# Optimization experiments

Measured on AMD Instinct MI355X. Metric: run time of the kernel, lower is better.

Reference implementation:

```python
import jax, jax.numpy as jnp
import numpy as np

HIDDEN = 768
FF = 3072
N_HEADS = 12
HEAD = HIDDEN // N_HEADS
WIDTH = 512  # attention window (number of attended keys, causal)
B, S = 2, 4096
EPS = 1e-6


def _rotary_sincos(seq_len, dim):
    # GPT-J style: freqs per pair, each value repeated twice (interleaved)
    inv_freq = 1.0 / (10000.0 ** (np.arange(0, dim, 2, dtype=np.float32) / dim))
    t = np.arange(seq_len, dtype=np.float32)
    ang = np.einsum('s,d->sd', t, inv_freq)              # [S, dim/2]
    ang = np.repeat(ang, 2, axis=-1)                     # [S, dim]
    return jnp.asarray(np.sin(ang))[:, None, :], jnp.asarray(np.cos(ang))[:, None, :]


def setup_inputs() -> dict:
    key = jax.random.key(0)
    ks = jax.random.split(key, 4)
    x = jax.random.normal(ks[0], (B, S, HIDDEN), dtype=jnp.float32)
    sin, cos = _rotary_sincos(S, HEAD)                   # [S,1,HEAD] each
    W_in = jax.random.normal(ks[1], (HIDDEN, 3 * HIDDEN + FF), dtype=jnp.float32) / np.sqrt(HIDDEN)
    b_in = jnp.zeros((3 * HIDDEN + FF,), dtype=jnp.float32)
    W_out = jax.random.normal(ks[2], (HIDDEN + FF, HIDDEN), dtype=jnp.float32) / np.sqrt(HIDDEN + FF)
    b_out = jnp.zeros((HIDDEN,), dtype=jnp.float32)
    w_norm = jnp.ones((HIDDEN,), dtype=jnp.float32)
    return {"x": x, "sin": sin, "cos": cos, "w_norm": w_norm,
            "W_in": W_in, "b_in": b_in, "W_out": W_out, "b_out": b_out}


def _rotate_every_two(x):
    x1 = x[..., ::2]
    x2 = x[..., 1::2]
    return jnp.stack((-x2, x1), axis=-1).reshape(x.shape)


def _apply_rope(x, sin, cos):
    # x: [B,S,H,hd]; sin/cos: [S,1,hd] -> broadcast as [1,S,1,hd]
    sin = sin[None]
    cos = cos[None]
    return x * cos + _rotate_every_two(x) * sin


def _windowed_attention(q, k, v, width):
    # q,k,v: [B,S,H,hd]; causal local attention: key j valid iff 0 <= i-j < width
    b, s, h, d = q.shape
    wb = width  # block size == window; each query block attends blocks (b-1, b)
    nb = s // wb
    scale = 1.0 / np.sqrt(d)
    qb = q.reshape(b, nb, wb, h, d)
    kp = jnp.pad(k, ((0, 0), (wb, 0), (0, 0), (0, 0))).reshape(b, nb + 1, wb, h, d)
    vp = jnp.pad(v, ((0, 0), (wb, 0), (0, 0), (0, 0))).reshape(b, nb + 1, wb, h, d)
    kb = jnp.concatenate([kp[:, :-1], kp[:, 1:]], axis=2)   # [B,nb,2wb,H,hd]
    vb = jnp.concatenate([vp[:, :-1], vp[:, 1:]], axis=2)
    scores = jnp.einsum('bnqhd,bnkhd->bnhqk', qb, kb) * scale
    qi = jnp.arange(wb)
    ki = jnp.arange(2 * wb)
    bi = jnp.arange(nb)
    diff = wb + qi[:, None] - ki[None, :]                    # i - j per block
    base = (diff >= 0) & (diff < width)                      # [wb, 2wb]
    valid_j = (bi[:, None, None] >= 1) | (ki[None, None, :] >= wb)  # j >= 0
    mask = base[None] & valid_j                              # [nb, wb, 2wb]
    neg = jnp.finfo(scores.dtype).min
    scores = jnp.where(mask[None, :, None], scores, neg)
    p = jax.nn.softmax(scores, axis=-1)
    out = jnp.einsum('bnhqk,bnkhd->bnqhd', p, vb)
    return out.reshape(b, s, h * d)


def reference(x, sin, cos, w_norm, W_in, b_in, W_out, b_out):
    # RMSNorm
    ms = jnp.mean(x * x, axis=-1, keepdims=True)
    xn = x * jax.lax.rsqrt(ms + EPS) * w_norm
    # fused QKV + FF projection
    t = xn @ W_in + b_in                                     # [B,S,3*HIDDEN+FF]
    ff = t[:, :, -FF:]
    qkv = t[:, :, :-FF].reshape(x.shape[0], x.shape[1], 3, N_HEADS, HEAD)
    q = _apply_rope(qkv[:, :, 0], sin, cos)
    k = _apply_rope(qkv[:, :, 1], sin, cos)
    v = qkv[:, :, 2]
    attn = _windowed_attention(q, k, v, WIDTH)               # [B,S,HIDDEN]
    ff = jax.nn.gelu(ff, approximate=False)
    combined = jnp.concatenate((attn, ff), axis=-1)          # [B,S,HIDDEN+FF]
    return combined @ W_out + b_out
```

## Files before the change

kernel.cpp:

```cpp
#include <hip/hip_runtime.h>
#include <hip/hip_bf16.h>

typedef short bf16x8 __attribute__((ext_vector_type(8)));
typedef float f32x4 __attribute__((ext_vector_type(4)));

#define LOG2E 1.4426950408889634f
#define QKV_E ((size_t)24*4096*64)

__device__ __forceinline__ float bfu2f(unsigned short u) {
  unsigned v = ((unsigned)u) << 16;
  return __builtin_bit_cast(float, v);
}
__device__ __forceinline__ unsigned short f2bfu(float f) {
  unsigned u = __builtin_bit_cast(unsigned, f);
  u += 0x7fffu + ((u >> 16) & 1u);
  return (unsigned short)(u >> 16);
}
__device__ __forceinline__ unsigned packbf2(float lo, float hi) {
  return (unsigned)f2bfu(lo) | ((unsigned)f2bfu(hi) << 16);
}
__device__ __forceinline__ float gelu_f(float v) {
  float a = fabsf(v) * 0.70710678118654752f;
  float t = 1.0f / (1.0f + 0.3275911f * a);
  float poly = ((((1.061405429f * t - 1.453152027f) * t + 1.421413741f) * t
                 - 0.284496736f) * t + 0.254829592f) * t;
  float erfa = 1.0f - poly * __expf(-a * a);
  float erfv = v >= 0.0f ? erfa : -erfa;
  return 0.5f * v * (1.0f + erfv);
}
__device__ __forceinline__ void gl_lds16(const ushort* g, ushort* l) {
  __builtin_amdgcn_global_load_lds(
      (const __attribute__((address_space(1))) unsigned int*)(const void*)g,
      (__attribute__((address_space(3))) unsigned int*)(void*)l, 16, 0, 0);
}

__global__ __launch_bounds__(256) void rmsnorm_k(const float* __restrict__ x,
    const float* __restrict__ w, ushort* __restrict__ xn) {
  int row = blockIdx.x, t = threadIdx.x;
  const float* xr = x + (size_t)row * 768;
  float v0 = xr[t], v1 = xr[t + 256], v2 = xr[t + 512];
  float ss = v0 * v0 + v1 * v1 + v2 * v2;
#pragma unroll
  for (int m = 32; m >= 1; m >>= 1) ss += __shfl_xor(ss, m, 64);
  __shared__ float part[4];
  if ((t & 63) == 0) part[t >> 6] = ss;
  __syncthreads();
  float tot = part[0] + part[1] + part[2] + part[3];
  float rr = rsqrtf(tot * (1.0f / 768.0f) + 1e-6f);
  ushort* xo = xn + (size_t)row * 768;
  xo[t]       = f2bfu(v0 * rr * w[t]);
  xo[t + 256] = f2bfu(v1 * rr * w[t + 256]);
  xo[t + 512] = f2bfu(v2 * rr * w[t + 512]);
}

__global__ __launch_bounds__(256) void tcvt_k(const float* __restrict__ in,
    ushort* __restrict__ out, int R, int C) {
  __shared__ float tile[32][33];
  int c0 = blockIdx.x * 32, r0 = blockIdx.y * 32;
  int t = threadIdx.x;
  int j = t & 31, i0 = t >> 5;
#pragma unroll
  for (int i = i0; i < 32; i += 8) tile[i][j] = in[(size_t)(r0 + i) * C + c0 + j];
  __syncthreads();
#pragma unroll
  for (int i = i0; i < 32; i += 8) out[(size_t)(c0 + i) * R + r0 + j] = f2bfu(tile[j][i]);
}

__global__ __launch_bounds__(256) void gemm1_k(const ushort* __restrict__ A,
    const ushort* __restrict__ Bt, const float* __restrict__ bias,
    const float* __restrict__ sn, const float* __restrict__ cs,
    ushort* __restrict__ qbuf, ushort* __restrict__ kbuf,
    ushort* __restrict__ vt, ushort* __restrict__ comb) {
  __shared__ __align__(16) ushort lds[2][2][128 * 64];
  const int t = threadIdx.x, lane = t & 63, w = t >> 6;
  const int wr = w >> 1, wc = w & 1;
  int bid = blockIdx.x;
  int n = (bid & 7) * 336 + (bid >> 3);
  int bx = n % 42, by = n / 42;
  const int mBase = by * 128, nBase = bx * 128;

  size_t gA[4], gB[4];
  int ldst[4];
#pragma unroll
  for (int j = 0; j < 4; ++j) {
    int row = w * 32 + j * 8 + (lane >> 3);
    int gc = ((lane & 7) ^ (lane >> 3)) * 8;
    gA[j] = (size_t)(mBase + row) * 768 + gc;
    gB[j] = (size_t)(nBase + row) * 768 + gc;
    ldst[j] = (w * 32 + j * 8) * 64;
  }

  f32x4 acc[4][4];
  f32x4 z = {0.f, 0.f, 0.f, 0.f};
#pragma unroll
  for (int m = 0; m < 4; ++m)
#pragma unroll
    for (int nn = 0; nn < 4; ++nn) acc[m][nn] = z;

#pragma unroll
  for (int j = 0; j < 4; ++j) {
    gl_lds16(A + gA[j], &lds[0][0][0] + ldst[j]);
    gl_lds16(Bt + gB[j], &lds[0][1][0] + ldst[j]);
  }
  __syncthreads();

#pragma unroll 1
  for (int kt = 0; kt < 12; ++kt) {
    const int cur = kt & 1;
    if (kt < 11) {
      int k0 = (kt + 1) * 64;
#pragma unroll
      for (int j = 0; j < 4; ++j) {
        gl_lds16(A + gA[j] + k0, &lds[1 - cur][0][0] + ldst[j]);
        gl_lds16(Bt + gB[j] + k0, &lds[1 - cur][1][0] + ldst[j]);
      }
    }
    const ushort* As = &lds[cur][0][0];
    const ushort* Bs = &lds[cur][1][0];
#pragma unroll
    for (int kk = 0; kk < 2; ++kk) {
      bf16x8 af[4], bff[4];
#pragma unroll
      for (int m = 0; m < 4; ++m) {
        int row = wr * 64 + m * 16 + (lane & 15);
        int slot = (kk * 4 + (lane >> 4)) ^ (lane & 7);
        af[m] = *(const bf16x8*)(As + row * 64 + slot * 8);
      }
#pragma unroll
      for (int nn = 0; nn < 4; ++nn) {
        int row = wc * 64 + nn * 16 + (lane & 15);
        int slot = (kk * 4 + (lane >> 4)) ^ (lane & 7);
        bff[nn] = *(const bf16x8*)(Bs + row * 64 + slot * 8);
      }
#pragma unroll
      for (int m = 0; m < 4; ++m)
#pragma unroll
        for (int nn = 0; nn < 4; ++nn)
          acc[m][nn] = __builtin_amdgcn_mfma_f32_16x16x32_bf16(bff[nn], af[m], acc[m][nn], 0, 0, 0);
    }
    __syncthreads();
  }

  const bool isff = (nBase >= 2304);
  const int region = nBase / 768;
#pragma unroll
  for (int m = 0; m < 4; ++m) {
    int row = mBase + wr * 64 + m * 16 + (lane & 15);
    int b = row >> 12, s = row & 4095;
#pragma unroll
    for (int nn = 0; nn < 4; ++nn) {
      int col = nBase + wc * 64 + nn * 16 + ((lane >> 4) << 2);
      f32x4 v = acc[m][nn] + *(const f32x4*)(bias + col);
      if (isff) {
        ushort4 o;
        o.x = f2bfu(gelu_f(v[0]));
        o.y = f2bfu(gelu_f(v[1]));
        o.z = f2bfu(gelu_f(v[2]));
        o.w = f2bfu(gelu_f(v[3]));
        *(ushort4*)(comb + (size_t)row * 3840 + (col - 1536)) = o;
      } else {
        int rem = col - region * 768;
        int h = rem >> 6, d0 = rem & 63;
        if (region == 2) {
          int l = s & 127;
          int pnn = l >> 4, pg = (l >> 2) & 3, pr = l & 3;
          int sp = (s & ~127) | (((pnn >> 1) * 4 + pg) * 8 + (pnn & 1) * 4 + pr);
          size_t vb = (size_t)((b * 12 + h) * 64 + d0) * 4096 + sp;
          vt[vb]          = f2bfu(v[0]);
          vt[vb + 4096]   = f2bfu(v[1]);
          vt[vb + 2*4096] = f2bfu(v[2]);
          vt[vb + 3*4096] = f2bfu(v[3]);
        } else {
          f32x4 sv = *(const f32x4*)(sn + (s << 6) + d0);
          f32x4 cv = *(const f32x4*)(cs + (s << 6) + d0);
          float o0 = v[0] * cv[0] - v[1] * sv[0];
          float o1 = v[1] * cv[0] + v[0] * sv[0];
          float o2 = v[2] * cv[2] - v[3] * sv[2];
          float o3 = v[3] * cv[2] + v[2] * sv[2];
          ushort4 o;
          if (region == 0) {
            o.x = f2bfu(o0 * 0.125f); o.y = f2bfu(o1 * 0.125f);
            o.z = f2bfu(o2 * 0.125f); o.w = f2bfu(o3 * 0.125f);
            *(ushort4*)(qbuf + ((size_t)((b * 12 + h) * 4096 + s)) * 64 + d0) = o;
          } else {
            o.x = f2bfu(o0); o.y = f2bfu(o1); o.z = f2bfu(o2); o.w = f2bfu(o3);
            *(ushort4*)(kbuf + ((size_t)((b * 12 + h) * 4096 + s)) * 64 + d0) = o;
          }
        }
      }
    }
  }
}

__global__ __launch_bounds__(512) void gemm2_k(const ushort* __restrict__ A,
    const ushort* __restrict__ Bt, const float* __restrict__ bias,
    float* __restrict__ out) {
  __shared__ __align__(16) ushort lds[2][2][2][128 * 64];
  const int t = threadIdx.x;
  const int grp = t >> 8, tl = t & 255;
  const int lane = tl & 63, w4 = tl >> 6;
  const int wr = w4 >> 1, wc = w4 & 1;
  int bid = blockIdx.x;
  int n = (bid & 7) * 48 + (bid >> 3);
  int bx = n % 6, by = n / 6;
  const int mBase = by * 128, nBase = bx * 128;
  const int kOff = grp * 1920;

  size_t gA[4], gB[4];
  int ldst[4];
#pragma unroll
  for (int j = 0; j < 4; ++j) {
    int row = w4 * 32 + j * 8 + (lane >> 3);
    int gc = ((lane & 7) ^ (lane >> 3)) * 8;
    gA[j] = (size_t)(mBase + row) * 3840 + kOff + gc;
    gB[j] = (size_t)(nBase + row) * 3840 + kOff + gc;
    ldst[j] = (w4 * 32 + j * 8) * 64;
  }

  f32x4 acc[4][4];
  f32x4 z = {0.f, 0.f, 0.f, 0.f};
#pragma unroll
  for (int m = 0; m < 4; ++m)
#pragma unroll
    for (int nn = 0; nn < 4; ++nn) acc[m][nn] = z;

#pragma unroll
  for (int j = 0; j < 4; ++j) {
    gl_lds16(A + gA[j], &lds[grp][0][0][0] + ldst[j]);
    gl_lds16(Bt + gB[j], &lds[grp][0][1][0] + ldst[j]);
  }
  __syncthreads();

#pragma unroll 1
  for (int kt = 0; kt < 30; ++kt) {
    const int cur = kt & 1;
    if (kt < 29) {
      int k0 = (kt + 1) * 64;
#pragma unroll
      for (int j = 0; j < 4; ++j) {
        gl_lds16(A + gA[j] + k0, &lds[grp][1 - cur][0][0] + ldst[j]);
        gl_lds16(Bt + gB[j] + k0, &lds[grp][1 - cur][1][0] + ldst[j]);
      }
    }
    const ushort* As = &lds[grp][cur][0][0];
    const ushort* Bs = &lds[grp][cur][1][0];
#pragma unroll
    for (int kk = 0; kk < 2; ++kk) {
      bf16x8 af[4], bff[4];
#pragma unroll
      for (int m = 0; m < 4; ++m) {
        int row = wr * 64 + m * 16 + (lane & 15);
        int slot = (kk * 4 + (lane >> 4)) ^ (lane & 7);
        af[m] = *(const bf16x8*)(As + row * 64 + slot * 8);
      }
#pragma unroll
      for (int nn = 0; nn < 4; ++nn) {
        int row = wc * 64 + nn * 16 + (lane & 15);
        int slot = (kk * 4 + (lane >> 4)) ^ (lane & 7);
        bff[nn] = *(const bf16x8*)(Bs + row * 64 + slot * 8);
      }
#pragma unroll
      for (int m = 0; m < 4; ++m)
#pragma unroll
        for (int nn = 0; nn < 4; ++nn)
          acc[m][nn] = __builtin_amdgcn_mfma_f32_16x16x32_bf16(bff[nn], af[m], acc[m][nn], 0, 0, 0);
    }
    __syncthreads();
  }

  f32x4* sc = (f32x4*)&lds[1][0][0][0];
  if (grp == 1) {
#pragma unroll
    for (int m = 0; m < 4; ++m)
#pragma unroll
      for (int nn = 0; nn < 4; ++nn) sc[tl * 16 + m * 4 + nn] = acc[m][nn];
  }
  __syncthreads();
  if (grp == 0) {
#pragma unroll
    for (int m = 0; m < 4; ++m) {
      int row = mBase + wr * 64 + m * 16 + (lane & 15);
#pragma unroll
      for (int nn = 0; nn < 4; ++nn) {
        int col = nBase + wc * 64 + nn * 16 + ((lane >> 4) << 2);
        f32x4 v = acc[m][nn] + sc[tl * 16 + m * 4 + nn] + *(const f32x4*)(bias + col);
        *(f32x4*)(out + (size_t)row * 768 + col) = v;
      }
    }
  }
}

__global__ __launch_bounds__(256, 2) void attn_k(const ushort* __restrict__ qb,
    const ushort* __restrict__ kb, const ushort* __restrict__ vt,
    ushort* __restrict__ comb) {
  __shared__ __align__(16) ushort KS[2][128 * 64];
  __shared__ __align__(16) ushort VS[2][64 * 128];
  int bid = blockIdx.x;
  int nb = (bid & 7) * 96 + (bid >> 3);
  int qt = nb & 31, bh = nb >> 5;
  const int t = threadIdx.x, lane = t & 63, w = t >> 6;
  const int g = lane >> 4, q15 = lane & 15;
  const int qlo = qt * 128;
  const size_t base = (size_t)bh * 4096 * 64;

  size_t kSrc[4], vSrc[4];
  int dstOff[4];
#pragma unroll
  for (int j = 0; j < 4; ++j) {
    int ck = (w * 4 + j) * 64 + lane;
    int key = ck >> 3, sl = ck & 7;
    kSrc[j] = (size_t)key * 64 + ((sl ^ (key & 7)) << 3);
    int dd = ck >> 4, s16 = ck & 15;
    vSrc[j] = (size_t)dd * 4096 + ((s16 ^ (dd & 15)) << 3);
    dstOff[j] = (w * 4 + j) * 512;
  }

  bf16x8 qa[2][2];
#pragma unroll
  for (int m = 0; m < 2; ++m)
#pragma unroll
    for (int kk = 0; kk < 2; ++kk) {
      int row = qlo + w * 32 + m * 16 + q15;
      qa[m][kk] = *(const bf16x8*)(qb + base + (size_t)row * 64 + kk * 32 + g * 8);
    }

  f32x4 z = {0.f, 0.f, 0.f, 0.f};
  f32x4 o[2][4];
#pragma unroll
  for (int m = 0; m < 2; ++m)
#pragma unroll
    for (int df = 0; df < 4; ++df) o[m][df] = z;
  float m_run[2] = {-1e30f, -1e30f}, l_run[2] = {0.f, 0.f};

  const int t0 = qt >= 4 ? qt - 4 : 0;
  const int nt = qt - t0 + 1;
  {
    int k0 = t0 * 128;
#pragma unroll
    for (int j = 0; j < 4; ++j) {
      gl_lds16(kb + base + (size_t)k0 * 64 + kSrc[j], &KS[0][0] + dstOff[j]);
      gl_lds16(vt + base + k0 + vSrc[j], &VS[0][0] + dstOff[j]);
    }
  }
  __syncthreads();

  const int qrow0 = qlo + w * 32 + q15;
#pragma unroll 1
  for (int it = 0; it < nt; ++it) {
    const int kt = t0 + it, k0 = kt * 128, cur = it & 1;
    if (it + 1 < nt) {
      int k1 = k0 + 128;
#pragma unroll
      for (int j = 0; j < 4; ++j) {
        gl_lds16(kb + base + (size_t)k1 * 64 + kSrc[j], &KS[1 - cur][0] + dstOff[j]);
        gl_lds16(vt + base + k1 + vSrc[j], &VS[1 - cur][0] + dstOff[j]);
      }
    }
    f32x4 s[2][8];
#pragma unroll
    for (int m = 0; m < 2; ++m)
#pragma unroll
      for (int nn = 0; nn < 8; ++nn) s[m][nn] = z;
#pragma unroll
    for (int kk = 0; kk < 2; ++kk) {
      bf16x8 kf[8];
#pragma unroll
      for (int nn = 0; nn < 8; ++nn) {
        int row = nn * 16 + q15;
        int slot = (kk * 4 + g) ^ (q15 & 7);
        kf[nn] = *(const bf16x8*)(&KS[cur][0] + row * 64 + slot * 8);
      }
#pragma unroll
      for (int m = 0; m < 2; ++m)
#pragma unroll
        for (int nn = 0; nn < 8; ++nn)
          s[m][nn] = __builtin_amdgcn_mfma_f32_16x16x32_bf16(kf[nn], qa[m][kk], s[m][nn], 0, 0, 0);
    }
    if (kt == qt) {
#pragma unroll
      for (int m = 0; m < 2; ++m) {
        int ql = qrow0 + m * 16 - k0;
#pragma unroll
        for (int nn = 0; nn < 8; ++nn)
#pragma unroll
          for (int r = 0; r < 4; ++r)
            if (nn * 16 + g * 4 + r > ql) s[m][nn][r] = -3e38f;
      }
    } else if (kt == qt - 4) {
#pragma unroll
      for (int m = 0; m < 2; ++m) {
        int ql = qrow0 + m * 16 - k0;
#pragma unroll
        for (int nn = 0; nn < 8; ++nn)
#pragma unroll
          for (int r = 0; r < 4; ++r)
            if (ql - (nn * 16 + g * 4 + r) >= 512) s[m][nn][r] = -3e38f;
      }
    }
    float mx[2];
    bool need = false;
#pragma unroll
    for (int m = 0; m < 2; ++m) {
      float v = s[m][0][0];
#pragma unroll
      for (int nn = 0; nn < 8; ++nn)
#pragma unroll
        for (int r = 0; r < 4; ++r) v = fmaxf(v, s[m][nn][r]);
      v = fmaxf(v, __shfl_xor(v, 16, 64));
      v = fmaxf(v, __shfl_xor(v, 32, 64));
      mx[m] = v;
      need |= (v > m_run[m] + 8.f);
    }
    if (__any(need)) {
#pragma unroll
      for (int m = 0; m < 2; ++m) {
        float mn = fmaxf(m_run[m], mx[m]);
        float sc = exp2f((m_run[m] - mn) * LOG2E);
        m_run[m] = mn;
        l_run[m] *= sc;
#pragma unroll
        for (int df = 0; df < 4; ++df) o[m][df] *= sc;
      }
    }
#pragma unroll
    for (int m = 0; m < 2; ++m) {
      float mr = m_run[m];
      float ls = 0.f;
#pragma unroll
      for (int nn = 0; nn < 8; ++nn)
#pragma unroll
        for (int r = 0; r < 4; ++r) {
          float p = exp2f((s[m][nn][r] - mr) * LOG2E);
          s[m][nn][r] = p;
          ls += p;
        }
      ls += __shfl_xor(ls, 16, 64);
      ls += __shfl_xor(ls, 32, 64);
      l_run[m] += ls;
    }
#pragma unroll
    for (int kk2 = 0; kk2 < 4; ++kk2) {
      bf16x8 pa[2];
#pragma unroll
      for (int m = 0; m < 2; ++m) {
        int4 pi4;
        pi4.x = (int)packbf2(s[m][2*kk2][0],   s[m][2*kk2][1]);
        pi4.y = (int)packbf2(s[m][2*kk2][2],   s[m][2*kk2][3]);
        pi4.z = (int)packbf2(s[m][2*kk2+1][0], s[m][2*kk2+1][1]);
        pi4.w = (int)packbf2(s[m][2*kk2+1][2], s[m][2*kk2+1][3]);
        pa[m] = __builtin_bit_cast(bf16x8, pi4);
      }
#pragma unroll
      for (int df = 0; df < 4; ++df) {
        int row = df * 16 + q15;
        int slot = (kk2 * 4 + g) ^ q15;
        bf16x8 vf = *(const bf16x8*)(&VS[cur][0] + row * 128 + slot * 8);
#pragma unroll
        for (int m = 0; m < 2; ++m)
          o[m][df] = __builtin_amdgcn_mfma_f32_16x16x32_bf16(vf, pa[m], o[m][df], 0, 0, 0);
      }
    }
    __syncthreads();
  }

  int b = bh / 12, h = bh % 12;
#pragma unroll
  for (int m = 0; m < 2; ++m) {
    float inv = 1.0f / l_run[m];
    int row = qrow0 + m * 16;
#pragma unroll
    for (int df = 0; df < 4; ++df) {
      ushort4 ov;
      ov.x = f2bfu(o[m][df][0] * inv);
      ov.y = f2bfu(o[m][df][1] * inv);
      ov.z = f2bfu(o[m][df][2] * inv);
      ov.w = f2bfu(o[m][df][3] * inv);
      *(ushort4*)(comb + (size_t)(b * 4096 + row) * 3840 + h * 64 + df * 16 + g * 4) = ov;
    }
  }
}

extern "C" void kernel_launch(void* const* d_in, const int* in_sizes, int n_in,
                              void* d_out, int out_size, void* d_ws, size_t ws_size,
                              hipStream_t stream) {
  (void)in_sizes; (void)n_in; (void)out_size; (void)ws_size;
  const float* x      = (const float*)d_in[0];
  const float* sin_t  = (const float*)d_in[1];
  const float* cos_t  = (const float*)d_in[2];
  const float* w_norm = (const float*)d_in[3];
  const float* W_in   = (const float*)d_in[4];
  const float* b_in   = (const float*)d_in[5];
  const float* W_out  = (const float*)d_in[6];
  const float* b_out  = (const float*)d_in[7];
  float* out = (float*)d_out;

  const size_t XN_E  = (size_t)8192 * 768;
  ushort* xn      = (ushort*)d_ws;
  ushort* qbuf    = xn + XN_E;
  ushort* kbuf    = qbuf + QKV_E;
  ushort* vt      = kbuf + QKV_E;
  ushort* w_in_t  = vt + QKV_E;
  ushort* w_out_t = w_in_t + (size_t)5376 * 768;
  ushort* comb    = w_out_t + (size_t)768 * 3840;

  rmsnorm_k<<<dim3(8192), dim3(256), 0, stream>>>(x, w_norm, xn);
  tcvt_k<<<dim3(5376 / 32, 768 / 32), dim3(256), 0, stream>>>(W_in, w_in_t, 768, 5376);
  tcvt_k<<<dim3(768 / 32, 3840 / 32), dim3(256), 0, stream>>>(W_out, w_out_t, 3840, 768);
  gemm1_k<<<dim3(2688), dim3(256), 0, stream>>>(xn, w_in_t, b_in, sin_t, cos_t,
                                                qbuf, kbuf, vt, comb);
  attn_k<<<dim3(768), dim3(256), 0, stream>>>(qbuf, kbuf, vt, comb);
  gemm2_k<<<dim3(384), dim3(512), 0, stream>>>(comb, w_out_t, b_out, out);
}
```

Baseline: 265.4 us.

## Overlap prefetch with compute via vmcnt waits, regroup tile mapping, drop gemm2 split-K

Replaces full __syncthreads in the double-buffered loops of gemm1, gemm2 and attention with explicit s_waitcnt vmcnt(8)/lgkmcnt(0) plus s_barrier. The async loads for the next tile can then stay in flight while the current tile is computed, instead of being drained at every barrier. Block-to-tile mapping for the GEMMs is changed to XCD-local groups for better L2 reuse, and gemm2 drops its intra-block split-K (512 threads, LDS reduction) for a 256-thread single-K kernel with occupancy hint 2. This trades parallelism per tile for lower LDS use and no reduction step, and it relies on the hand-counted vmcnt value being right.

```diff
diff --git a/kernel.cpp b/kernel.cpp
--- a/kernel.cpp
+++ b/kernel.cpp
@@ -33,6 +33,10 @@
       (const __attribute__((address_space(1))) unsigned int*)(const void*)g,
       (__attribute__((address_space(3))) unsigned int*)(void*)l, 16, 0, 0);
 }
+#define WAIT_VM8  asm volatile("s_waitcnt vmcnt(8)" ::: "memory")
+#define WAIT_VM0  asm volatile("s_waitcnt vmcnt(0)" ::: "memory")
+#define WAIT_LGKM asm volatile("s_waitcnt lgkmcnt(0)" ::: "memory")
+#define BAR       __builtin_amdgcn_s_barrier()
 
 __global__ __launch_bounds__(256) void rmsnorm_k(const float* __restrict__ x,
     const float* __restrict__ w, ushort* __restrict__ xn) {
@@ -66,7 +70,7 @@
   for (int i = i0; i < 32; i += 8) out[(size_t)(c0 + i) * R + r0 + j] = f2bfu(tile[j][i]);
 }
 
-__global__ __launch_bounds__(256) void gemm1_k(const ushort* __restrict__ A,
+__global__ __launch_bounds__(256, 2) void gemm1_k(const ushort* __restrict__ A,
     const ushort* __restrict__ Bt, const float* __restrict__ bias,
     const float* __restrict__ sn, const float* __restrict__ cs,
     ushort* __restrict__ qbuf, ushort* __restrict__ kbuf,
@@ -75,8 +79,10 @@
   const int t = threadIdx.x, lane = t & 63, w = t >> 6;
   const int wr = w >> 1, wc = w & 1;
   int bid = blockIdx.x;
-  int n = (bid & 7) * 336 + (bid >> 3);
-  int bx = n % 42, by = n / 42;
+  int xcd = bid & 7, local = bid >> 3;
+  int grp = local / 48, r6 = local % 48;
+  int bx = grp * 6 + r6 % 6;
+  int by = xcd * 8 + r6 / 6;
   const int mBase = by * 128, nBase = bx * 128;
 
   size_t gA[4], gB[4];
@@ -102,7 +108,6 @@
     gl_lds16(A + gA[j], &lds[0][0][0] + ldst[j]);
     gl_lds16(Bt + gB[j], &lds[0][1][0] + ldst[j]);
   }
-  __syncthreads();
 
 #pragma unroll 1
   for (int kt = 0; kt < 12; ++kt) {
@@ -114,7 +119,11 @@
         gl_lds16(A + gA[j] + k0, &lds[1 - cur][0][0] + ldst[j]);
         gl_lds16(Bt + gB[j] + k0, &lds[1 - cur][1][0] + ldst[j]);
       }
-    }
+      WAIT_VM8;
+    } else {
+      WAIT_VM0;
+    }
+    BAR;
     const ushort* As = &lds[cur][0][0];
     const ushort* Bs = &lds[cur][1][0];
 #pragma unroll
@@ -138,7 +147,8 @@
         for (int nn = 0; nn < 4; ++nn)
           acc[m][nn] = __builtin_amdgcn_mfma_f32_16x16x32_bf16(bff[nn], af[m], acc[m][nn], 0, 0, 0);
     }
-    __syncthreads();
+    WAIT_LGKM;
+    BAR;
   }
 
   const bool isff = (nBase >= 2304);
@@ -192,29 +202,28 @@
   }
 }
 
-__global__ __launch_bounds__(512) void gemm2_k(const ushort* __restrict__ A,
+__global__ __launch_bounds__(256, 2) void gemm2_k(const ushort* __restrict__ A,
     const ushort* __restrict__ Bt, const float* __restrict__ bias,
     float* __restrict__ out) {
-  __shared__ __align__(16) ushort lds[2][2][2][128 * 64];
-  const int t = threadIdx.x;
-  const int grp = t >> 8, tl = t & 255;
-  const int lane = tl & 63, w4 = tl >> 6;
-  const int wr = w4 >> 1, wc = w4 & 1;
+  __shared__ __align__(16) ushort lds[2][2][128 * 64];
+  const int t = threadIdx.x, lane = t & 63, w = t >> 6;
+  const int wr = w >> 1, wc = w & 1;
   int bid = blockIdx.x;
-  int n = (bid & 7) * 48 + (bid >> 3);
-  int bx = n % 6, by = n / 6;
+  int xcd = bid & 7, local = bid >> 3;
+  int g = local / 4, r4 = local % 4;
+  int bx = (g % 3) * 2 + (r4 & 1);
+  int by = xcd * 8 + (g / 3) * 2 + (r4 >> 1);
   const int mBase = by * 128, nBase = bx * 128;
-  const int kOff = grp * 1920;
 
   size_t gA[4], gB[4];
   int ldst[4];
 #pragma unroll
   for (int j = 0; j < 4; ++j) {
-    int row = w4 * 32 + j * 8 + (lane >> 3);
+    int row = w * 32 + j * 8 + (lane >> 3);
     int gc = ((lane & 7) ^ (lane >> 3)) * 8;
-    gA[j] = (size_t)(mBase + row) * 3840 + kOff + gc;
-    gB[j] = (size_t)(nBase + row) * 3840 + kOff + gc;
-    ldst[j] = (w4 * 32 + j * 8) * 64;
+    gA[j] = (size_t)(mBase + row) * 3840 + gc;
+    gB[j] = (size_t)(nBase + row) * 3840 + gc;
+    ldst[j] = (w * 32 + j * 8) * 64;
   }
 
   f32x4 acc[4][4];
@@ -226,24 +235,27 @@
 
 #pragma unroll
   for (int j = 0; j < 4; ++j) {
-    gl_lds16(A + gA[j], &lds[grp][0][0][0] + ldst[j]);
-    gl_lds16(Bt + gB[j], &lds[grp][0][1][0] + ldst[j]);
-  }
-  __syncthreads();
+    gl_lds16(A + gA[j], &lds[0][0][0] + ldst[j]);
+    gl_lds16(Bt + gB[j], &lds[0][1][0] + ldst[j]);
+  }
 
 #pragma unroll 1
-  for (int kt = 0; kt < 30; ++kt) {
+  for (int kt = 0; kt < 60; ++kt) {
     const int cur = kt & 1;
-    if (kt < 29) {
+    if (kt < 59) {
       int k0 = (kt + 1) * 64;
 #pragma unroll
       for (int j = 0; j < 4; ++j) {
-        gl_lds16(A + gA[j] + k0, &lds[grp][1 - cur][0][0] + ldst[j]);
-        gl_lds16(Bt + gB[j] + k0, &lds[grp][1 - cur][1][0] + ldst[j]);
-      }
-    }
-    const ushort* As = &lds[grp][cur][0][0];
-    const ushort* Bs = &lds[grp][cur][1][0];
+        gl_lds16(A + gA[j] + k0, &lds[1 - cur][0][0] + ldst[j]);
+        gl_lds16(Bt + gB[j] + k0, &lds[1 - cur][1][0] + ldst[j]);
+      }
+      WAIT_VM8;
+    } else {
+      WAIT_VM0;
+    }
+    BAR;
+    const ushort* As = &lds[cur][0][0];
+    const ushort* Bs = &lds[cur][1][0];
 #pragma unroll
     for (int kk = 0; kk < 2; ++kk) {
       bf16x8 af[4], bff[4];
@@ -265,27 +277,18 @@
         for (int nn = 0; nn < 4; ++nn)
           acc[m][nn] = __builtin_amdgcn_mfma_f32_16x16x32_bf16(bff[nn], af[m], acc[m][nn], 0, 0, 0);
     }
-    __syncthreads();
-  }
-
-  f32x4* sc = (f32x4*)&lds[1][0][0][0];
-  if (grp == 1) {
-#pragma unroll
-    for (int m = 0; m < 4; ++m)
-#pragma unroll
-      for (int nn = 0; nn < 4; ++nn) sc[tl * 16 + m * 4 + nn] = acc[m][nn];
-  }
-  __syncthreads();
-  if (grp == 0) {
-#pragma unroll
-    for (int m = 0; m < 4; ++m) {
-      int row = mBase + wr * 64 + m * 16 + (lane & 15);
-#pragma unroll
-      for (int nn = 0; nn < 4; ++nn) {
-        int col = nBase + wc * 64 + nn * 16 + ((lane >> 4) << 2);
-        f32x4 v = acc[m][nn] + sc[tl * 16 + m * 4 + nn] + *(const f32x4*)(bias + col);
-        *(f32x4*)(out + (size_t)row * 768 + col) = v;
-      }
+    WAIT_LGKM;
+    BAR;
+  }
+
+#pragma unroll
+  for (int m = 0; m < 4; ++m) {
+    int row = mBase + wr * 64 + m * 16 + (lane & 15);
+#pragma unroll
+    for (int nn = 0; nn < 4; ++nn) {
+      int col = nBase + wc * 64 + nn * 16 + ((lane >> 4) << 2);
+      f32x4 v = acc[m][nn] + *(const f32x4*)(bias + col);
+      *(f32x4*)(out + (size_t)row * 768 + col) = v;
     }
   }
 }
@@ -342,7 +345,6 @@
       gl_lds16(vt + base + k0 + vSrc[j], &VS[0][0] + dstOff[j]);
     }
   }
-  __syncthreads();
 
   const int qrow0 = qlo + w * 32 + q15;
 #pragma unroll 1
@@ -355,7 +357,11 @@
         gl_lds16(kb + base + (size_t)k1 * 64 + kSrc[j], &KS[1 - cur][0] + dstOff[j]);
         gl_lds16(vt + base + k1 + vSrc[j], &VS[1 - cur][0] + dstOff[j]);
       }
-    }
+      WAIT_VM8;
+    } else {
+      WAIT_VM0;
+    }
+    BAR;
     f32x4 s[2][8];
 #pragma unroll
     for (int m = 0; m < 2; ++m)
@@ -460,7 +466,8 @@
           o[m][df] = __builtin_amdgcn_mfma_f32_16x16x32_bf16(vf, pa[m], o[m][df], 0, 0, 0);
       }
     }
-    __syncthreads();
+    WAIT_LGKM;
+    BAR;
   }
 
   int b = bh / 12, h = bh % 12;
@@ -509,5 +516,5 @@
   gemm1_k<<<dim3(2688), dim3(256), 0, stream>>>(xn, w_in_t, b_in, sin_t, cos_t,
                                                 qbuf, kbuf, vt, comb);
   attn_k<<<dim3(768), dim3(256), 0, stream>>>(qbuf, kbuf, vt, comb);
-  gemm2_k<<<dim3(384), dim3(512), 0, stream>>>(comb, w_out_t, b_out, out);
-}
+  gemm2_k<<<dim3(384), dim3(256), 0, stream>>>(comb, w_out_t, b_out, out);
+}
```

After: 238.9 us. 10.0% less time.
